# Performance work log

Hardware: AMD Instinct MI355X
Metric: run time of the kernel (lower is better)

The kernel has to match this reference:

```python
import jax, jax.numpy as jnp
import numpy as np

B, T, C = 512, 128, 384   # batch, seq (== block_size), embed_dim
H, D = 6, 64              # n_heads, head_size
BLOCK_SIZE = 128


def setup_inputs() -> dict:
    key = jax.random.key(0)
    ks = jax.random.split(key, 6)
    s = C ** -0.5  # init scale, values irrelevant to correctness
    x = jax.random.normal(ks[0], (B, T, C), dtype=jnp.float32)
    Wq = jax.random.normal(ks[1], (H, C, D), dtype=jnp.float32) * s
    Wk = jax.random.normal(ks[2], (H, C, D), dtype=jnp.float32) * s
    Wv = jax.random.normal(ks[3], (H, C, D), dtype=jnp.float32) * s
    Wp = jax.random.normal(ks[4], (H * D, C), dtype=jnp.float32) * s
    bp = jax.random.normal(ks[5], (C,), dtype=jnp.float32) * 0.01
    return {"x": x, "Wq": Wq, "Wk": Wk, "Wv": Wv, "Wp": Wp, "bp": bp}


def reference(x, Wq, Wk, Wv, Wp, bp):
    # Forward of MultiHeadAttentionClass (eval mode: dropout disabled).
    # Heads are vectorized instead of the original Python per-head loop.
    Bx, Tx, Cx = x.shape
    x = x[:, :BLOCK_SIZE, :]                       # truncate to block_size
    t = x.shape[1]
    q = jnp.einsum('btc,hcd->bhtd', x, Wq)         # [B,H,T,D]
    k = jnp.einsum('btc,hcd->bhtd', x, Wk)
    v = jnp.einsum('btc,hcd->bhtd', x, Wv)
    scores = jnp.einsum('bhtd,bhsd->bhts', q, k) * (D ** -0.5)  # [B,H,T,T]
    causal = jnp.tril(jnp.ones((t, t), dtype=bool))
    scores = jnp.where(causal[None, None], scores, -jnp.inf)
    wei = jax.nn.softmax(scores, axis=-1)
    out = jnp.einsum('bhts,bhsd->bhtd', wei, v)    # [B,H,T,D]
    out = out.transpose(0, 2, 1, 3).reshape(x.shape[0], t, H * D)  # concat heads
    out = out @ Wp + bp                            # projection to embed_dim
    return out
```

## Files before the change

kernel.cpp:

```cpp
#include <hip/hip_runtime.h>

#define NB 512
#define NTOK 128
#define NC 384
#define NH 6
#define ND 64

typedef short s16x8 __attribute__((ext_vector_type(8)));
typedef float f32x4 __attribute__((ext_vector_type(4)));

#define MFMA16(a, b, c) __builtin_amdgcn_mfma_f32_16x16x32_bf16((a), (b), (c), 0, 0, 0)

static __device__ __forceinline__ unsigned short f2bf(float f) {
  unsigned int u = __builtin_bit_cast(unsigned int, f);
  u = (u + 0x7FFFu + ((u >> 16) & 1u)) >> 16;
  return (unsigned short)u;
}

static __device__ __forceinline__ uint2 pack4(float a, float b, float c, float d) {
  union { unsigned short h[4]; uint2 u; } t;
  t.h[0] = f2bf(a); t.h[1] = f2bf(b); t.h[2] = f2bf(c); t.h[3] = f2bf(d);
  return t.u;
}

static __device__ __forceinline__ s16x8 cvt8(float4 a, float4 b) {
  union { unsigned short h[8]; s16x8 v; } t;
  t.h[0] = f2bf(a.x); t.h[1] = f2bf(a.y); t.h[2] = f2bf(a.z); t.h[3] = f2bf(a.w);
  t.h[4] = f2bf(b.x); t.h[5] = f2bf(b.y); t.h[6] = f2bf(b.z); t.h[7] = f2bf(b.w);
  return t.v;
}

static __device__ __forceinline__ void g2l16(const void* g, void* l) {
  __builtin_amdgcn_global_load_lds(
      (const __attribute__((address_space(1))) unsigned int*)g,
      (__attribute__((address_space(3))) unsigned int*)l, 16, 0, 0);
}

#define XGRP 3145728
#define WGRP 55296
__global__ __launch_bounds__(256) void prep(
    const float* __restrict__ x, const float* __restrict__ Wq,
    const float* __restrict__ Wk, const float* __restrict__ Wv,
    const float* __restrict__ Wp,
    unsigned short* __restrict__ xbf, unsigned short* __restrict__ wimg,
    unsigned short* __restrict__ wpT) {
  int g = blockIdx.x * 256 + threadIdx.x;
  if (g < XGRP) {
    int cg = g & 3;
    int t = (g >> 2) & 127;
    int kc = (g >> 9) % 12;
    int b = g / 6144;
    const float* src = x + (((size_t)b * NTOK + t) * NC + kc * 32 + cg * 8);
    float4 f0 = *(const float4*)src;
    float4 f1 = *(const float4*)(src + 4);
    *(s16x8*)(xbf + (size_t)g * 8) = cvt8(f0, f1);
  } else if (g < XGRP + WGRP) {
    int gw = g - XGRP;
    int cg = gw & 3;
    int d = (gw >> 2) & 63;
    int rem = gw >> 8;
    int m = rem % 3;
    int hk = rem / 3;
    int kc = hk % 12;
    int h = hk / 12;
    const float* W = (m == 0) ? Wq : (m == 1) ? Wk : Wv;
    const float* s = W + ((size_t)h * NC + kc * 32 + cg * 8) * ND + d;
    union { unsigned short hh[8]; s16x8 v; } o;
#pragma unroll
    for (int j = 0; j < 8; ++j) o.hh[j] = f2bf(s[j * ND]);
    *(s16x8*)(wimg + (size_t)gw * 8) = o.v;
  } else {
    int j = g - XGRP - WGRP;
    int cc = j / 48;
    int rb = (j % 48) * 8;
    union { unsigned short hh[8]; s16x8 v; } o;
#pragma unroll
    for (int i = 0; i < 8; ++i) o.hh[i] = f2bf(Wp[(size_t)(rb + i) * NC + cc]);
    *(s16x8*)(wpT + (size_t)cc * NC + rb) = o.v;
  }
}

__global__ __launch_bounds__(512, 2) void attn_fused(
    const unsigned short* __restrict__ xbf, const unsigned short* __restrict__ wimg,
    unsigned short* __restrict__ O) {
  const int lbid = (blockIdx.x & 7) * 384 + (blockIdx.x >> 3);
  const int b = lbid / NH;
  const int h = lbid % NH;
  const int tid = threadIdx.x;
  const int lane = tid & 63;
  const int l15 = lane & 15;
  const int lg = lane >> 4;
  const int wid = tid >> 6;
  const int r0 = wid * 16;
  const int mw = wid & 3;
  const int nw = wid >> 2;

  __shared__ __align__(16) union {
    char dbuf[2][20480];
    struct { unsigned short qs[128][72]; unsigned short ks[128][72]; } qk;
    unsigned short pB[128][136];
  } u;
  __shared__ __align__(16) unsigned short vts[64][136];

  f32x4 acc[3][2][2];
#pragma unroll
  for (int m = 0; m < 3; ++m)
#pragma unroll
    for (int i = 0; i < 2; ++i)
#pragma unroll
      for (int j = 0; j < 2; ++j) acc[m][i][j] = f32x4{0.f, 0.f, 0.f, 0.f};

  const char* xsrc = (const char*)xbf + (size_t)b * 98304;
  const char* wsrc = (const char*)wimg + (size_t)h * 147456;
  const int o16 = tid * 16;

#define STAGE(kc, pg)                                                   \
  {                                                                     \
    const char* sx = xsrc + (kc) * 8192;                                \
    const char* sw = wsrc + (kc) * 12288;                               \
    char* db = u.dbuf[pg];                                              \
    g2l16(sx + o16, db + o16);                                          \
    g2l16(sw + o16, db + 8192 + o16);                                   \
    if (tid < 256) g2l16(sw + 8192 + o16, db + 16384 + o16);            \
  }

  STAGE(0, 0);
  for (int kc = 0; kc < 12; ++kc) {
    __syncthreads();
    if (kc < 11) STAGE(kc + 1, (kc + 1) & 1);
    const char* cb = u.dbuf[kc & 1];
    const unsigned short* xs = (const unsigned short*)cb;
    const unsigned short* wl = (const unsigned short*)(cb + 8192);
    s16x8 a0 = *(const s16x8*)(xs + (mw * 32 + l15) * 32 + lg * 8);
    s16x8 a1 = *(const s16x8*)(xs + (mw * 32 + 16 + l15) * 32 + lg * 8);
#pragma unroll
    for (int m = 0; m < 3; ++m)
#pragma unroll
      for (int nt2 = 0; nt2 < 2; ++nt2) {
        s16x8 bm = *(const s16x8*)(wl + (m * 64 + nw * 32 + nt2 * 16 + l15) * 32 + lg * 8);
        acc[m][nt2][0] = MFMA16(a0, bm, acc[m][nt2][0]);
        acc[m][nt2][1] = MFMA16(a1, bm, acc[m][nt2][1]);
      }
  }

  __syncthreads();
#pragma unroll
  for (int nt2 = 0; nt2 < 2; ++nt2)
#pragma unroll
    for (int mt = 0; mt < 2; ++mt) {
      const int row = mw * 32 + mt * 16 + 4 * lg;
      const int col = nw * 32 + nt2 * 16 + l15;
#pragma unroll
      for (int r = 0; r < 4; ++r) {
        u.qk.qs[row + r][col] = f2bf(acc[0][nt2][mt][r] * 0.125f);
        u.qk.ks[row + r][col] = f2bf(acc[1][nt2][mt][r]);
      }
      *(uint2*)&vts[col][row] =
          pack4(acc[2][nt2][mt][0], acc[2][nt2][mt][1],
                acc[2][nt2][mt][2], acc[2][nt2][mt][3]);
    }
  __syncthreads();

  f32x4 sacc[8];
#pragma unroll
  for (int j = 0; j < 8; ++j) sacc[j] = f32x4{0.f, 0.f, 0.f, 0.f};

#pragma unroll
  for (int kd = 0; kd < 2; ++kd) {
    s16x8 bq = *(const s16x8*)&u.qk.qs[r0 + l15][kd * 32 + lg * 8];
#pragma unroll
    for (int nt = 0; nt < 8; ++nt) {
      if (nt <= wid) {
        s16x8 ak = *(const s16x8*)&u.qk.ks[nt * 16 + l15][kd * 32 + lg * 8];
        sacc[nt] = MFMA16(ak, bq, sacc[nt]);
      }
    }
  }

  const int q = r0 + l15;
  float mx = -1e30f;
#pragma unroll
  for (int nt = 0; nt < 8; ++nt) {
    if (nt <= wid) {
#pragma unroll
      for (int r = 0; r < 4; ++r) {
        int s = nt * 16 + 4 * lg + r;
        float v = (s <= q) ? sacc[nt][r] : -1e30f;
        sacc[nt][r] = v;
        mx = fmaxf(mx, v);
      }
    }
  }
  mx = fmaxf(mx, __shfl_xor(mx, 16, 64));
  mx = fmaxf(mx, __shfl_xor(mx, 32, 64));
  float sm = 0.f;
#pragma unroll
  for (int nt = 0; nt < 8; ++nt) {
    if (nt <= wid) {
#pragma unroll
      for (int r = 0; r < 4; ++r) {
        float e = __expf(sacc[nt][r] - mx);
        sacc[nt][r] = e;
        sm += e;
      }
    }
  }
  sm += __shfl_xor(sm, 16, 64);
  sm += __shfl_xor(sm, 32, 64);
  float inv = 1.f / sm;

  __syncthreads();
#pragma unroll
  for (int nt = 0; nt < 8; ++nt) {
    uint2 pv;
    if (nt <= wid)
      pv = pack4(sacc[nt][0] * inv, sacc[nt][1] * inv, sacc[nt][2] * inv, sacc[nt][3] * inv);
    else { pv.x = 0u; pv.y = 0u; }
    *(uint2*)&u.pB[r0 + l15][nt * 16 + 4 * lg] = pv;
  }
  __syncthreads();

  f32x4 oacc[4];
#pragma unroll
  for (int j = 0; j < 4; ++j) oacc[j] = f32x4{0.f, 0.f, 0.f, 0.f};
#pragma unroll
  for (int kd = 0; kd < 4; ++kd) {
    if (kd * 32 <= r0 + 15) {
      s16x8 bp = *(const s16x8*)&u.pB[r0 + l15][kd * 32 + lg * 8];
#pragma unroll
      for (int dt = 0; dt < 4; ++dt) {
        s16x8 av = *(const s16x8*)&vts[dt * 16 + l15][kd * 32 + lg * 8];
        oacc[dt] = MFMA16(av, bp, oacc[dt]);
      }
    }
  }

  unsigned short* Op = O + ((size_t)(b * NTOK) + r0 + l15) * (NH * ND) + h * ND;
#pragma unroll
  for (int dt = 0; dt < 4; ++dt)
    *(uint2*)&Op[dt * 16 + 4 * lg] =
        pack4(oacc[dt][0], oacc[dt][1], oacc[dt][2], oacc[dt][3]);
}

__global__ __launch_bounds__(256, 2) void proj_gemm(
    const unsigned short* __restrict__ O, const unsigned short* __restrict__ wpT,
    const float* __restrict__ bp, float* __restrict__ out) {
  const int ntile = blockIdx.x >> 9;
  const int mtile = blockIdx.x & 511;
  const int m0 = mtile * 128, n0 = ntile * 128;
  const int tid = threadIdx.x;
  const int lane = tid & 63;
  const int l15 = lane & 15, lg = lane >> 4;
  const int r0 = (tid >> 6) * 32;

  __shared__ __align__(16) char db[2][32768];

  f32x4 acc[2][8];
#pragma unroll
  for (int i = 0; i < 2; ++i)
#pragma unroll
    for (int j = 0; j < 8; ++j) acc[i][j] = f32x4{0.f, 0.f, 0.f, 0.f};

  const char* Ab = (const char*)O + (size_t)m0 * (NC * 2);
  const char* Bb = (const char*)wpT + (size_t)n0 * (NC * 2);

#define PSTAGE(kc, pg)                                                       \
  {                                                                          \
    char* dd = db[pg];                                                       \
    _Pragma("unroll")                                                        \
    for (int i = 0; i < 4; ++i) {                                            \
      int d = i * 4096 + tid * 16;                                           \
      int kd = d >> 13, row = (d >> 6) & 127, cg = (d >> 4) & 3;             \
      size_t so = ((size_t)row * NC + (kc) * 64 + kd * 32 + cg * 8) * 2;     \
      g2l16(Ab + so, dd + d);                                                \
      g2l16(Bb + so, dd + 16384 + d);                                        \
    }                                                                        \
  }

  PSTAGE(0, 0);
  for (int kc = 0; kc < 6; ++kc) {
    __syncthreads();
    if (kc < 5) PSTAGE(kc + 1, (kc + 1) & 1);
    const unsigned short* A = (const unsigned short*)db[kc & 1];
    const unsigned short* B = (const unsigned short*)(db[kc & 1] + 16384);
#pragma unroll
    for (int kd = 0; kd < 2; ++kd) {
      const unsigned short* Ak = A + kd * 4096;
      const unsigned short* Bk = B + kd * 4096;
      s16x8 a0 = *(const s16x8*)(Ak + (r0 + l15) * 32 + lg * 8);
      s16x8 a1 = *(const s16x8*)(Ak + (r0 + 16 + l15) * 32 + lg * 8);
#pragma unroll
      for (int nt = 0; nt < 8; ++nt) {
        s16x8 bb = *(const s16x8*)(Bk + (nt * 16 + l15) * 32 + lg * 8);
        acc[0][nt] = MFMA16(a0, bb, acc[0][nt]);
        acc[1][nt] = MFMA16(a1, bb, acc[1][nt]);
      }
    }
  }
#pragma unroll
  for (int mt = 0; mt < 2; ++mt)
#pragma unroll
    for (int nt = 0; nt < 8; ++nt) {
      int trow = m0 + r0 + 16 * mt + 4 * lg;
      int col = n0 + nt * 16 + l15;
      float bias = bp[col];
#pragma unroll
      for (int r = 0; r < 4; ++r)
        out[(size_t)(trow + r) * NC + col] = acc[mt][nt][r] + bias;
    }
}

extern "C" void kernel_launch(void* const* d_in, const int* in_sizes, int n_in,
                              void* d_out, int out_size, void* d_ws, size_t ws_size,
                              hipStream_t stream) {
  const float* x  = (const float*)d_in[0];
  const float* Wq = (const float*)d_in[1];
  const float* Wk = (const float*)d_in[2];
  const float* Wv = (const float*)d_in[3];
  const float* Wp = (const float*)d_in[4];
  const float* bp = (const float*)d_in[5];
  float* out = (float*)d_out;

  char* ws = (char*)d_ws;
  unsigned short* O    = (unsigned short*)(ws);
  unsigned short* wimg = (unsigned short*)(ws + 50331648);
  unsigned short* wpT  = (unsigned short*)(ws + 51216384);
  unsigned short* xbf  = (unsigned short*)d_out;

  prep<<<12576, 256, 0, stream>>>(x, Wq, Wk, Wv, Wp, xbf, wimg, wpT);
  attn_fused<<<NB * NH, 512, 0, stream>>>(xbf, wimg, O);
  proj_gemm<<<3 * 512, 256, 0, stream>>>(O, wpT, bp, out);
}
```

Baseline: 362.1 us.

## Swizzle LDS layouts, triple-buffer attention QKV loads, retile projection GEMM

The prep kernel now writes x and the QKV weights with an XOR swizzle of 8-element groups, so the MFMA fragment reads in attention avoid LDS bank conflicts. The QKV projection loop switches to a three-stage buffer with explicit vmcnt waits and raw barriers, plus setprio around the MFMAs. The output projection GEMM is retiled to 256x128 tiles with 512 threads, 32-wide K steps, swizzled LDS, an XCD-aware block remap and setprio. The gains in LDS efficiency and latency hiding come at the cost of more LDS use and hand-tuned wait counts that must exactly match the number of outstanding loads.

```diff
diff --git a/kernel.cpp b/kernel.cpp
--- a/kernel.cpp
+++ b/kernel.cpp
@@ -35,6 +35,8 @@
       (const __attribute__((address_space(1))) unsigned int*)g,
       (__attribute__((address_space(3))) unsigned int*)l, 16, 0, 0);
 }
+
+#define FENCE() asm volatile("" ::: "memory")
 
 #define XGRP 3145728
 #define WGRP 55296
@@ -50,7 +52,8 @@
     int t = (g >> 2) & 127;
     int kc = (g >> 9) % 12;
     int b = g / 6144;
-    const float* src = x + (((size_t)b * NTOK + t) * NC + kc * 32 + cg * 8);
+    int gl = cg ^ (t & 3);
+    const float* src = x + (((size_t)b * NTOK + t) * NC + kc * 32 + gl * 8);
     float4 f0 = *(const float4*)src;
     float4 f1 = *(const float4*)(src + 4);
     *(s16x8*)(xbf + (size_t)g * 8) = cvt8(f0, f1);
@@ -64,7 +67,8 @@
     int kc = hk % 12;
     int h = hk / 12;
     const float* W = (m == 0) ? Wq : (m == 1) ? Wk : Wv;
-    const float* s = W + ((size_t)h * NC + kc * 32 + cg * 8) * ND + d;
+    int gl = cg ^ (d & 3);
+    const float* s = W + ((size_t)h * NC + kc * 32 + gl * 8) * ND + d;
     union { unsigned short hh[8]; s16x8 v; } o;
 #pragma unroll
     for (int j = 0; j < 8; ++j) o.hh[j] = f2bf(s[j * ND]);
@@ -94,9 +98,10 @@
   const int r0 = wid * 16;
   const int mw = wid & 3;
   const int nw = wid >> 2;
+  const int xswz = (lg ^ (l15 & 3)) * 8;
 
   __shared__ __align__(16) union {
-    char dbuf[2][20480];
+    char dbuf[3][20480];
     struct { unsigned short qs[128][72]; unsigned short ks[128][72]; } qk;
     unsigned short pB[128][136];
   } u;
@@ -114,33 +119,41 @@
   const char* wsrc = (const char*)wimg + (size_t)h * 147456;
   const int o16 = tid * 16;
 
-#define STAGE(kc, pg)                                                   \
+#define STAGE(kc)                                                       \
   {                                                                     \
     const char* sx = xsrc + (kc) * 8192;                                \
     const char* sw = wsrc + (kc) * 12288;                               \
-    char* db = u.dbuf[pg];                                              \
+    char* db = u.dbuf[(kc) % 3];                                        \
     g2l16(sx + o16, db + o16);                                          \
     g2l16(sw + o16, db + 8192 + o16);                                   \
     if (tid < 256) g2l16(sw + 8192 + o16, db + 16384 + o16);            \
   }
 
-  STAGE(0, 0);
+  STAGE(0);
+  STAGE(1);
+#pragma unroll
   for (int kc = 0; kc < 12; ++kc) {
-    __syncthreads();
-    if (kc < 11) STAGE(kc + 1, (kc + 1) & 1);
-    const char* cb = u.dbuf[kc & 1];
+    if (kc == 11) { asm volatile("s_waitcnt vmcnt(0)" ::: "memory"); }
+    else if (wid < 4) { asm volatile("s_waitcnt vmcnt(3)" ::: "memory"); }
+    else { asm volatile("s_waitcnt vmcnt(2)" ::: "memory"); }
+    __builtin_amdgcn_s_barrier();
+    FENCE();
+    if (kc < 10) STAGE(kc + 2);
+    const char* cb = u.dbuf[kc % 3];
     const unsigned short* xs = (const unsigned short*)cb;
     const unsigned short* wl = (const unsigned short*)(cb + 8192);
-    s16x8 a0 = *(const s16x8*)(xs + (mw * 32 + l15) * 32 + lg * 8);
-    s16x8 a1 = *(const s16x8*)(xs + (mw * 32 + 16 + l15) * 32 + lg * 8);
+    s16x8 a0 = *(const s16x8*)(xs + (mw * 32 + l15) * 32 + xswz);
+    s16x8 a1 = *(const s16x8*)(xs + (mw * 32 + 16 + l15) * 32 + xswz);
+    __builtin_amdgcn_s_setprio(1);
 #pragma unroll
     for (int m = 0; m < 3; ++m)
 #pragma unroll
       for (int nt2 = 0; nt2 < 2; ++nt2) {
-        s16x8 bm = *(const s16x8*)(wl + (m * 64 + nw * 32 + nt2 * 16 + l15) * 32 + lg * 8);
+        s16x8 bm = *(const s16x8*)(wl + (m * 64 + nw * 32 + nt2 * 16 + l15) * 32 + xswz);
         acc[m][nt2][0] = MFMA16(a0, bm, acc[m][nt2][0]);
         acc[m][nt2][1] = MFMA16(a1, bm, acc[m][nt2][1]);
       }
+    __builtin_amdgcn_s_setprio(0);
   }
 
   __syncthreads();
@@ -242,67 +255,76 @@
         pack4(oacc[dt][0], oacc[dt][1], oacc[dt][2], oacc[dt][3]);
 }
 
-__global__ __launch_bounds__(256, 2) void proj_gemm(
+__global__ __launch_bounds__(512, 2) void proj_gemm(
     const unsigned short* __restrict__ O, const unsigned short* __restrict__ wpT,
     const float* __restrict__ bp, float* __restrict__ out) {
-  const int ntile = blockIdx.x >> 9;
-  const int mtile = blockIdx.x & 511;
-  const int m0 = mtile * 128, n0 = ntile * 128;
+  const int lb = (blockIdx.x & 7) * 96 + (blockIdx.x >> 3);
+  const int nt3 = lb >> 8;
+  const int mtile = lb & 255;
+  const int m0 = mtile * 256, n0 = nt3 * 128;
   const int tid = threadIdx.x;
   const int lane = tid & 63;
   const int l15 = lane & 15, lg = lane >> 4;
-  const int r0 = (tid >> 6) * 32;
-
-  __shared__ __align__(16) char db[2][32768];
-
-  f32x4 acc[2][8];
-#pragma unroll
-  for (int i = 0; i < 2; ++i)
-#pragma unroll
-    for (int j = 0; j < 8; ++j) acc[i][j] = f32x4{0.f, 0.f, 0.f, 0.f};
+  const int wid = tid >> 6;
+  const int mw4 = wid & 3;
+  const int nw = wid >> 2;
+  const int xswz = (lg ^ (l15 & 3)) * 8;
+
+  __shared__ __align__(16) char db[2][24576];
+
+  f32x4 acc[4][4];
+#pragma unroll
+  for (int i = 0; i < 4; ++i)
+#pragma unroll
+    for (int j = 0; j < 4; ++j) acc[i][j] = f32x4{0.f, 0.f, 0.f, 0.f};
 
   const char* Ab = (const char*)O + (size_t)m0 * (NC * 2);
   const char* Bb = (const char*)wpT + (size_t)n0 * (NC * 2);
 
-#define PSTAGE(kc, pg)                                                       \
-  {                                                                          \
-    char* dd = db[pg];                                                       \
-    _Pragma("unroll")                                                        \
-    for (int i = 0; i < 4; ++i) {                                            \
-      int d = i * 4096 + tid * 16;                                           \
-      int kd = d >> 13, row = (d >> 6) & 127, cg = (d >> 4) & 3;             \
-      size_t so = ((size_t)row * NC + (kc) * 64 + kd * 32 + cg * 8) * 2;     \
-      g2l16(Ab + so, dd + d);                                                \
-      g2l16(Bb + so, dd + 16384 + d);                                        \
-    }                                                                        \
+#define PSTAGE(kc, pg)                                                        \
+  {                                                                           \
+    char* dd = db[pg];                                                        \
+    _Pragma("unroll")                                                         \
+    for (int i = 0; i < 2; ++i) {                                             \
+      int s = tid + i * 512;                                                  \
+      int r = s >> 2, cg = s & 3;                                             \
+      size_t so = ((size_t)r * NC + (kc) * 32 + ((cg ^ (r & 3)) * 8)) * 2;    \
+      g2l16(Ab + so, dd + s * 16);                                            \
+    }                                                                         \
+    {                                                                         \
+      int r = tid >> 2, cg = tid & 3;                                         \
+      size_t so = ((size_t)r * NC + (kc) * 32 + ((cg ^ (r & 3)) * 8)) * 2;    \
+      g2l16(Bb + so, dd + 16384 + tid * 16);                                  \
+    }                                                                         \
   }
 
   PSTAGE(0, 0);
-  for (int kc = 0; kc < 6; ++kc) {
+  for (int kc = 0; kc < 12; ++kc) {
     __syncthreads();
-    if (kc < 5) PSTAGE(kc + 1, (kc + 1) & 1);
+    if (kc < 11) PSTAGE(kc + 1, (kc + 1) & 1);
     const unsigned short* A = (const unsigned short*)db[kc & 1];
     const unsigned short* B = (const unsigned short*)(db[kc & 1] + 16384);
-#pragma unroll
-    for (int kd = 0; kd < 2; ++kd) {
-      const unsigned short* Ak = A + kd * 4096;
-      const unsigned short* Bk = B + kd * 4096;
-      s16x8 a0 = *(const s16x8*)(Ak + (r0 + l15) * 32 + lg * 8);
-      s16x8 a1 = *(const s16x8*)(Ak + (r0 + 16 + l15) * 32 + lg * 8);
-#pragma unroll
-      for (int nt = 0; nt < 8; ++nt) {
-        s16x8 bb = *(const s16x8*)(Bk + (nt * 16 + l15) * 32 + lg * 8);
-        acc[0][nt] = MFMA16(a0, bb, acc[0][nt]);
-        acc[1][nt] = MFMA16(a1, bb, acc[1][nt]);
-      }
-    }
-  }
-#pragma unroll
-  for (int mt = 0; mt < 2; ++mt)
-#pragma unroll
-    for (int nt = 0; nt < 8; ++nt) {
-      int trow = m0 + r0 + 16 * mt + 4 * lg;
-      int col = n0 + nt * 16 + l15;
+    s16x8 af[4], bf[4];
+#pragma unroll
+    for (int mt = 0; mt < 4; ++mt)
+      af[mt] = *(const s16x8*)(A + (mw4 * 64 + mt * 16 + l15) * 32 + xswz);
+#pragma unroll
+    for (int nt = 0; nt < 4; ++nt)
+      bf[nt] = *(const s16x8*)(B + (nw * 64 + nt * 16 + l15) * 32 + xswz);
+    __builtin_amdgcn_s_setprio(1);
+#pragma unroll
+    for (int mt = 0; mt < 4; ++mt)
+#pragma unroll
+      for (int nt = 0; nt < 4; ++nt)
+        acc[mt][nt] = MFMA16(af[mt], bf[nt], acc[mt][nt]);
+    __builtin_amdgcn_s_setprio(0);
+  }
+#pragma unroll
+  for (int mt = 0; mt < 4; ++mt)
+#pragma unroll
+    for (int nt = 0; nt < 4; ++nt) {
+      int trow = m0 + mw4 * 64 + mt * 16 + 4 * lg;
+      int col = n0 + nw * 64 + nt * 16 + l15;
       float bias = bp[col];
 #pragma unroll
       for (int r = 0; r < 4; ++r)
@@ -329,5 +351,5 @@
 
   prep<<<12576, 256, 0, stream>>>(x, Wq, Wk, Wv, Wp, xbf, wimg, wpT);
   attn_fused<<<NB * NH, 512, 0, stream>>>(xbf, wimg, O);
-  proj_gemm<<<3 * 512, 256, 0, stream>>>(O, wpT, bp, out);
-}
+  proj_gemm<<<768, 512, 0, stream>>>(O, wpT, bp, out);
+}
```

Result: faster. 354.5 us (-2.1%).
